# Kernel optimization log

Hardware: AMD Instinct MI355X
Metric: run time of the kernel (lower is better)

## Reference

```python
import jax, jax.numpy as jnp
import numpy as np
import math

B, T, D_MODEL, H = 2, 2048, 1024, 16
HD = D_MODEL // H  # head_dim = 64


def setup_inputs() -> dict:
    key = jax.random.key(0)
    ks = jax.random.split(key, 9)
    inp = {
        "x_q": jax.random.normal(ks[0], (B, T, D_MODEL), dtype=jnp.float32),
        "x_k": jax.random.normal(ks[1], (B, T, D_MODEL), dtype=jnp.float32),
        "x_v": jax.random.normal(ks[2], (B, T, D_MODEL), dtype=jnp.float32),
        "mask": jax.random.randint(ks[3], (B, T), 0, 2, dtype=jnp.int32),
        "causal": 1,
        "relative_position_bias": jax.random.normal(ks[4], (1, H, T, T), dtype=jnp.float32),
        "Wq": jax.random.normal(ks[5], (D_MODEL, D_MODEL), dtype=jnp.float32) * 0.02,
        "Wk": jax.random.normal(ks[6], (D_MODEL, D_MODEL), dtype=jnp.float32) * 0.02,
        "Wv": jax.random.normal(ks[7], (D_MODEL, D_MODEL), dtype=jnp.float32) * 0.02,
        "Wo": jax.random.normal(ks[8], (D_MODEL, D_MODEL), dtype=jnp.float32) * 0.02,
    }
    return inp


def _split_heads(x):
    b, t, _ = x.shape
    return x.reshape(b, t, H, HD).transpose(0, 2, 1, 3)  # (B, H, T, HD)


def reference(x_q, x_k, x_v, mask, causal, relative_position_bias, Wq, Wk, Wv, Wo):
    # torch.nn.Linear: y = x @ W.T
    q = _split_heads(x_q @ Wq.T)
    k = _split_heads(x_k @ Wk.T)
    v = _split_heads(x_v @ Wv.T)

    # padding mask (B, T_k) -> (B, 1, 1, T_k), combined with causal tril
    attn_mask = mask[:, None, None, :]
    if causal:
        tril = jnp.tril(jnp.ones((T, T), dtype=jnp.int32))[None, None]
        attn_mask = attn_mask & tril

    scores = jnp.einsum('bhqd,bhkd->bhqk', q, k) / math.sqrt(HD)
    scores = scores + relative_position_bias
    scores = jnp.where(attn_mask == 0, jnp.float32(-1e9), scores)
    attn = jax.nn.softmax(scores, axis=-1)  # (B, H, Tq, Tk)

    out_h = jnp.einsum('bhqk,bhkd->bhqd', attn, v)
    out = out_h.transpose(0, 2, 1, 3).reshape(B, T, D_MODEL)
    out = out @ Wo.T
    return out, attn
```

## Files before the change

kernel.cpp:

```cpp
#include <hip/hip_runtime.h>
#include <hip/hip_bf16.h>
#include <hip/hip_fp16.h>

#define B_ 2
#define T_ 2048
#define DM 1024
#define H_ 16
#define HD_ 64

typedef __attribute__((ext_vector_type(8))) short bf16x8v;
typedef __attribute__((ext_vector_type(4))) short short4v;
typedef __attribute__((ext_vector_type(4))) float f32x4;

__device__ __forceinline__ short f2bf(float f){
  unsigned u = __builtin_bit_cast(unsigned, f);
  u += 0x7fffu + ((u >> 16) & 1u);
  return (short)(u >> 16);
}
__device__ __forceinline__ float bf2f(short s){
  unsigned u = ((unsigned)(unsigned short)s) << 16;
  return __builtin_bit_cast(float, u);
}
__device__ __forceinline__ short f2h(float f){
  return __builtin_bit_cast(short, __float2half(f));
}
__device__ __forceinline__ float h2f(short s){
  return __half2float(__builtin_bit_cast(__half, s));
}

#define GLOAD_LDS16(g, l) \
  __builtin_amdgcn_global_load_lds((const __attribute__((address_space(1))) unsigned int*)(g), \
                                   (__attribute__((address_space(3))) unsigned int*)(l), 16, 0, 0)

#define MFMA16(a, b, c) __builtin_amdgcn_mfma_f32_16x16x32_bf16((a), (b), (c), 0, 0, 0)

__global__ __launch_bounds__(256) void conv_kernel(
    const float* __restrict__ s0, const float* __restrict__ s1, const float* __restrict__ s2,
    const float* __restrict__ s3, const float* __restrict__ s4, const float* __restrict__ s5,
    const float* __restrict__ s6,
    short* __restrict__ d0, short* __restrict__ d1, short* __restrict__ d2,
    short* __restrict__ d3, short* __restrict__ d4, short* __restrict__ d5,
    short* __restrict__ d6)
{
  int y = blockIdx.y;
  const float* s; short* d; int n;
  switch (y) {
    case 0: s = s0; d = d0; n = B_*T_*DM; break;
    case 1: s = s1; d = d1; n = B_*T_*DM; break;
    case 2: s = s2; d = d2; n = B_*T_*DM; break;
    case 3: s = s3; d = d3; n = DM*DM;   break;
    case 4: s = s4; d = d4; n = DM*DM;   break;
    case 5: s = s5; d = d5; n = DM*DM;   break;
    default: s = s6; d = d6; n = DM*DM;  break;
  }
  int i = (blockIdx.x * 256 + threadIdx.x) * 4;
  if (i >= n) return;
  float4 f = *(const float4*)(s + i);
  short4v o;
  o.x = f2bf(f.x); o.y = f2bf(f.y); o.z = f2bf(f.z); o.w = f2bf(f.w);
  *(short4v*)(d + i) = o;
}

__global__ __launch_bounds__(256) void proj_gemm(
    const short* __restrict__ xq, const short* __restrict__ xk, const short* __restrict__ xv,
    const short* __restrict__ wq, const short* __restrict__ wk, const short* __restrict__ wv,
    short* __restrict__ qo, short* __restrict__ ko, short* __restrict__ vto)
{
  __shared__ short As[128 * 32];
  __shared__ short Bs[128 * 32];
  const int z = blockIdx.z;
  const short* A  = (z == 0) ? xq : (z == 1) ? xk : xv;
  const short* Bw = (z == 0) ? wq : (z == 1) ? wk : wv;
  const int m0 = blockIdx.x * 128;
  const int n0 = blockIdx.y * 128;
  const int tid = threadIdx.x;
  const int w = tid >> 6, l = tid & 63;
  const int wr = w >> 1, wc = w & 1;
  const int fr = l & 15, kq8 = (l >> 4) * 8;
  const int srow = tid >> 2, scol = (tid & 3) * 8;

  f32x4 acc[4][4] = {};

  for (int k0 = 0; k0 < DM; k0 += 32) {
    __syncthreads();
    GLOAD_LDS16(A  + (size_t)(m0 + srow) * DM + k0 + scol,      (char*)As + tid * 16);
    GLOAD_LDS16(A  + (size_t)(m0 + 64 + srow) * DM + k0 + scol, (char*)As + 4096 + tid * 16);
    GLOAD_LDS16(Bw + (size_t)(n0 + srow) * DM + k0 + scol,      (char*)Bs + tid * 16);
    GLOAD_LDS16(Bw + (size_t)(n0 + 64 + srow) * DM + k0 + scol, (char*)Bs + 4096 + tid * 16);
    __syncthreads();
    bf16x8v a[4], b[4];
#pragma unroll
    for (int i = 0; i < 4; i++) a[i] = *(const bf16x8v*)&As[(wr * 64 + i * 16 + fr) * 32 + kq8];
#pragma unroll
    for (int j = 0; j < 4; j++) b[j] = *(const bf16x8v*)&Bs[(wc * 64 + j * 16 + fr) * 32 + kq8];
#pragma unroll
    for (int i = 0; i < 4; i++)
#pragma unroll
      for (int j = 0; j < 4; j++)
        acc[i][j] = MFMA16(a[i], b[j], acc[i][j]);
  }

  const float scale = (z == 0) ? 0.125f : 1.0f;
  short* dst01 = (z == 0) ? qo : ko;
#pragma unroll
  for (int i = 0; i < 4; i++) {
#pragma unroll
    for (int j = 0; j < 4; j++) {
#pragma unroll
      for (int r = 0; r < 4; r++) {
        int row = m0 + wr * 64 + i * 16 + (l >> 4) * 4 + r;
        int col = n0 + wc * 64 + j * 16 + fr;
        int bb = row >> 11, tt = row & (T_ - 1);
        int hh = col >> 6,  hd = col & (HD_ - 1);
        short v = f2bf(acc[i][j][r] * scale);
        if (z == 2)
          vto[(((size_t)bb * H_ + hh) * HD_ + hd) * T_ + tt] = v;
        else
          dst01[(((size_t)bb * H_ + hh) * T_ + tt) * HD_ + hd] = v;
      }
    }
  }
}

__global__ __launch_bounds__(256) void vsum_kernel(const short* __restrict__ vt,
                                                   float* __restrict__ vs)
{
  __shared__ float red[256];
  int bh = blockIdx.x;
  int tid = threadIdx.x;
  int hd = tid & 63, part = tid >> 6;
  const short* src = vt + ((size_t)bh * HD_ + hd) * T_ + part * 512;
  float s = 0.f;
  for (int i = 0; i < 512; i += 4) {
    short4v v = *(const short4v*)(src + i);
    s += bf2f(v.x) + bf2f(v.y) + bf2f(v.z) + bf2f(v.w);
  }
  red[tid] = s;
  __syncthreads();
  if (part == 0)
    vs[(size_t)bh * HD_ + hd] = red[hd] + red[64 + hd] + red[128 + hd] + red[192 + hd];
}

__global__ __launch_bounds__(512) void attn_kernel(
    const short* __restrict__ qw, const short* __restrict__ kw, const short* __restrict__ vt,
    const float* __restrict__ bias, const int* __restrict__ mask,
    const int* __restrict__ causal_p, const float* __restrict__ vsum,
    float* __restrict__ attn_out, short* __restrict__ outh)
{
  __shared__ short s_lds[32 * 2048];
  __shared__ unsigned char mk_lds[2 * T_];
  __shared__ float m_lds[32], l_lds[32];

  const int h  = blockIdx.y;
  const int q0 = blockIdx.x * 16;
  const int tid = threadIdx.x;
  const int w = tid >> 6, l = tid & 63;
  const int causal = *causal_p;
  const int L = causal ? (q0 + 16) : T_;
  const int Lpad = (L + 31) & ~31;
  const int fr = l & 15, kq8 = (l >> 4) * 8;

  for (int i = tid; i < 2 * T_; i += 512)
    mk_lds[i] = (unsigned char)(mask[i] != 0);
  __syncthreads();

  {
    bf16x8v qf[2][2];
#pragma unroll
    for (int b = 0; b < 2; b++)
#pragma unroll
      for (int ks = 0; ks < 2; ks++)
        qf[b][ks] = *(const bf16x8v*)&qw[(((size_t)b * H_ + h) * T_ + q0 + fr) * HD_ + ks * 32 + kq8];

    for (int nt = 0; nt < 16; ++nt) {
      int k0 = (nt * 8 + w) * 16;
      if (k0 >= L) break;
      f32x4 acc0 = {0.f, 0.f, 0.f, 0.f}, acc1 = {0.f, 0.f, 0.f, 0.f};
      {
        const short* kb0 = &kw[(((size_t)0 * H_ + h) * T_ + k0 + fr) * HD_ + kq8];
        acc0 = MFMA16(qf[0][0], *(const bf16x8v*)kb0, acc0);
        acc0 = MFMA16(qf[0][1], *(const bf16x8v*)(kb0 + 32), acc0);
        const short* kb1 = &kw[(((size_t)1 * H_ + h) * T_ + k0 + fr) * HD_ + kq8];
        acc1 = MFMA16(qf[1][0], *(const bf16x8v*)kb1, acc1);
        acc1 = MFMA16(qf[1][1], *(const bf16x8v*)(kb1 + 32), acc1);
      }
      int colg = k0 + fr;
      const float* bp = bias + ((size_t)h * T_ + q0 + (l >> 4) * 4) * T_ + colg;
      unsigned char mk0 = mk_lds[colg], mk1 = mk_lds[T_ + colg];
#pragma unroll
      for (int r = 0; r < 4; r++) {
        int qrel = (l >> 4) * 4 + r;
        float bi = bp[r * T_];
        bool cok = (!causal) || (colg <= q0 + qrel);
        float s0 = (mk0 && cok) ? (acc0[r] + bi) : -1e9f;
        float s1 = (mk1 && cok) ? (acc1[r] + bi) : -1e9f;
        int row0 = qrel, row1 = 16 + qrel;
        *(short*)((char*)s_lds + ((row0 * 4096 + colg * 2) ^ ((row0 & 7) << 4))) = f2h(s0);
        *(short*)((char*)s_lds + ((row1 * 4096 + colg * 2) ^ ((row1 & 7) << 4))) = f2h(s1);
      }
    }
  }
  __syncthreads();

  {
    int row = tid >> 4, j = tid & 15;
    float mx = -3e38f;
    for (int c = j * 8; c < L; c += 128) {
      int byte = (row * 4096 + c * 2) ^ ((row & 7) << 4);
      bf16x8v v = *(const bf16x8v*)((char*)s_lds + byte);
#pragma unroll
      for (int i = 0; i < 8; i++) mx = fmaxf(mx, h2f(v[i]));
    }
#pragma unroll
    for (int off = 1; off < 16; off <<= 1) mx = fmaxf(mx, __shfl_xor(mx, off));
    float sm = 0.f;
    for (int c = j * 8; c < L; c += 128) {
      int byte = (row * 4096 + c * 2) ^ ((row & 7) << 4);
      bf16x8v v = *(const bf16x8v*)((char*)s_lds + byte);
#pragma unroll
      for (int i = 0; i < 8; i++) sm += __expf(h2f(v[i]) - mx);
    }
#pragma unroll
    for (int off = 1; off < 16; off <<= 1) sm += __shfl_xor(sm, off);
    if (j == 0) { m_lds[row] = mx; l_lds[row] = sm; }
  }
  __syncthreads();

  {
    int row = tid >> 4, j = tid & 15;
    int b = row >> 4, qg = q0 + (row & 15);
    float mx = m_lds[row];
    bool fullmask = (mx <= -0.5e9f);
    float inv = fullmask ? 0.f : (1.0f / l_lds[row]);
    float fillv = fullmask ? (1.0f / (float)T_) : 0.f;
    float* arow = attn_out + (((size_t)b * H_ + h) * T_ + qg) * T_;
    for (int c = j * 8; c < Lpad; c += 128) {
      int byte = (row * 4096 + c * 2) ^ ((row & 7) << 4);
      if (c < L) {
        bf16x8v v = *(const bf16x8v*)((char*)s_lds + byte);
        float p[8];
#pragma unroll
        for (int i = 0; i < 8; i++)
          p[i] = fullmask ? 0.f : __expf(h2f(v[i]) - mx) * inv;
        float4 o0 = make_float4(fullmask ? fillv : p[0], fullmask ? fillv : p[1],
                                fullmask ? fillv : p[2], fullmask ? fillv : p[3]);
        float4 o1 = make_float4(fullmask ? fillv : p[4], fullmask ? fillv : p[5],
                                fullmask ? fillv : p[6], fullmask ? fillv : p[7]);
        *(float4*)(arow + c)     = o0;
        *(float4*)(arow + c + 4) = o1;
        bf16x8v pb;
#pragma unroll
        for (int i = 0; i < 8; i++) pb[i] = f2bf(p[i]);
        *(bf16x8v*)((char*)s_lds + byte) = pb;
      } else {
        bf16x8v zz = {0, 0, 0, 0, 0, 0, 0, 0};
        *(bf16x8v*)((char*)s_lds + byte) = zz;
      }
    }
    for (int c = L + j * 8; c < T_; c += 128) {
      float4 f4 = make_float4(fillv, fillv, fillv, fillv);
      *(float4*)(arow + c)     = f4;
      *(float4*)(arow + c + 4) = f4;
    }
  }
  __syncthreads();

  {
    int bsel = w >> 2;
    int hd0  = (w & 3) * 16;
    f32x4 acc = {0.f, 0.f, 0.f, 0.f};
    const short* vb = vt + (((size_t)bsel * H_ + h) * HD_ + hd0 + fr) * T_;
    for (int k0 = 0; k0 < Lpad; k0 += 32) {
      int arow = bsel * 16 + fr;
      int byte = (arow * 4096 + (k0 + kq8) * 2) ^ ((arow & 7) << 4);
      bf16x8v pa = *(const bf16x8v*)((char*)s_lds + byte);
      bf16x8v vv = *(const bf16x8v*)(vb + k0 + kq8);
      acc = MFMA16(pa, vv, acc);
    }
#pragma unroll
    for (int r = 0; r < 4; r++) {
      int qrel = (l >> 4) * 4 + r;
      int row = bsel * 16 + qrel;
      int hd = hd0 + fr;
      float val = acc[r];
      if (m_lds[row] <= -0.5e9f)
        val = vsum[((size_t)bsel * H_ + h) * HD_ + hd] * (1.0f / (float)T_);
      outh[(((size_t)bsel * H_ + h) * T_ + q0 + qrel) * HD_ + hd] = f2bf(val);
    }
  }
}

__global__ __launch_bounds__(256) void out_gemm(
    const short* __restrict__ Ah, const short* __restrict__ Bw, float* __restrict__ Co)
{
  __shared__ short As[128 * 32];
  __shared__ short Bs[128 * 32];
  const int m0 = blockIdx.x * 128;
  const int n0 = blockIdx.y * 128;
  const int tid = threadIdx.x;
  const int w = tid >> 6, l = tid & 63;
  const int wr = w >> 1, wc = w & 1;
  const int fr = l & 15, kq8 = (l >> 4) * 8;
  const int srow = tid >> 2, scol = (tid & 3) * 8;

  f32x4 acc[4][4] = {};

  for (int k0 = 0; k0 < DM; k0 += 32) {
    __syncthreads();
    int kk = k0 + scol;
    int hh = kk >> 6, hd = kk & 63;
    {
      int m1 = m0 + srow;
      const short* src1 = Ah + (((size_t)(m1 >> 11) * H_ + hh) * T_ + (m1 & (T_ - 1))) * HD_ + hd;
      GLOAD_LDS16(src1, (char*)As + tid * 16);
      int m2 = m0 + 64 + srow;
      const short* src2 = Ah + (((size_t)(m2 >> 11) * H_ + hh) * T_ + (m2 & (T_ - 1))) * HD_ + hd;
      GLOAD_LDS16(src2, (char*)As + 4096 + tid * 16);
    }
    GLOAD_LDS16(Bw + (size_t)(n0 + srow) * DM + kk,      (char*)Bs + tid * 16);
    GLOAD_LDS16(Bw + (size_t)(n0 + 64 + srow) * DM + kk, (char*)Bs + 4096 + tid * 16);
    __syncthreads();
    bf16x8v a[4], b[4];
#pragma unroll
    for (int i = 0; i < 4; i++) a[i] = *(const bf16x8v*)&As[(wr * 64 + i * 16 + fr) * 32 + kq8];
#pragma unroll
    for (int j = 0; j < 4; j++) b[j] = *(const bf16x8v*)&Bs[(wc * 64 + j * 16 + fr) * 32 + kq8];
#pragma unroll
    for (int i = 0; i < 4; i++)
#pragma unroll
      for (int j = 0; j < 4; j++)
        acc[i][j] = MFMA16(a[i], b[j], acc[i][j]);
  }

#pragma unroll
  for (int i = 0; i < 4; i++)
#pragma unroll
    for (int j = 0; j < 4; j++)
#pragma unroll
      for (int r = 0; r < 4; r++) {
        int row = m0 + wr * 64 + i * 16 + (l >> 4) * 4 + r;
        int col = n0 + wc * 64 + j * 16 + fr;
        Co[(size_t)row * DM + col] = acc[i][j][r];
      }
}

extern "C" void kernel_launch(void* const* d_in, const int* in_sizes, int n_in,
                              void* d_out, int out_size, void* d_ws, size_t ws_size,
                              hipStream_t stream)
{
  const float* x_q  = (const float*)d_in[0];
  const float* x_k  = (const float*)d_in[1];
  const float* x_v  = (const float*)d_in[2];
  const int*   mask = (const int*)d_in[3];
  const int*   causal = (const int*)d_in[4];
  const float* bias = (const float*)d_in[5];
  const float* Wq   = (const float*)d_in[6];
  const float* Wk   = (const float*)d_in[7];
  const float* Wv   = (const float*)d_in[8];
  const float* Wo   = (const float*)d_in[9];

  char* ws = (char*)d_ws;
  const size_t XB = (size_t)B_ * T_ * DM * 2;
  const size_t WB = (size_t)DM * DM * 2;
  short* xq_b = (short*)(ws + 0 * XB);
  short* xk_b = (short*)(ws + 1 * XB);
  short* xv_b = (short*)(ws + 2 * XB);
  short* wq_b = (short*)(ws + 3 * XB + 0 * WB);
  short* wk_b = (short*)(ws + 3 * XB + 1 * WB);
  short* wv_b = (short*)(ws + 3 * XB + 2 * WB);
  short* wo_b = (short*)(ws + 3 * XB + 3 * WB);
  short* q_ws  = (short*)(ws + 3 * XB + 4 * WB);
  short* k_ws  = (short*)(ws + 4 * XB + 4 * WB);
  short* vt_ws = (short*)(ws + 5 * XB + 4 * WB);
  short* oh_ws = (short*)(ws + 6 * XB + 4 * WB);
  float* vs_ws = (float*)(ws + 7 * XB + 4 * WB);

  float* out0 = (float*)d_out;
  float* attn = out0 + (size_t)B_ * T_ * DM;

  conv_kernel<<<dim3(4096, 7, 1), 256, 0, stream>>>(
      x_q, x_k, x_v, Wq, Wk, Wv, Wo,
      xq_b, xk_b, xv_b, wq_b, wk_b, wv_b, wo_b);

  proj_gemm<<<dim3(32, 8, 3), 256, 0, stream>>>(
      xq_b, xk_b, xv_b, wq_b, wk_b, wv_b, q_ws, k_ws, vt_ws);

  vsum_kernel<<<dim3(32, 1, 1), 256, 0, stream>>>(vt_ws, vs_ws);

  attn_kernel<<<dim3(T_ / 16, H_, 1), 512, 0, stream>>>(
      q_ws, k_ws, vt_ws, bias, mask, causal, vs_ws, attn, oh_ws);

  out_gemm<<<dim3(32, 8, 1), 256, 0, stream>>>(oh_ws, wo_b, out0);
}
```

Before: 517.2 us.

## Retile attention per batch with 8 query rows, split PV over key halves

Each attention block now covers one batch and 8 query rows instead of both batches and 16 rows, which shrinks LDS use from about 128KB to about 32KB and launches 4x as many blocks. Each wave now owns one softmax row. The PV product is split across two key halves and reduced through LDS. Attention-probability stores become nontemporal. The aim is more blocks resident per CU and better overlap of the large attn write. In exchange, half of each 16-row MFMA is wasted on duplicated rows, and the shared bias rows are no longer reused across batches within one block.

```diff
diff --git a/kernel.cpp b/kernel.cpp
--- a/kernel.cpp
+++ b/kernel.cpp
@@ -141,100 +141,94 @@
     vs[(size_t)bh * HD_ + hd] = red[hd] + red[64 + hd] + red[128 + hd] + red[192 + hd];
 }
 
-__global__ __launch_bounds__(512) void attn_kernel(
+__global__ __launch_bounds__(512, 6) void attn_kernel(
     const short* __restrict__ qw, const short* __restrict__ kw, const short* __restrict__ vt,
     const float* __restrict__ bias, const int* __restrict__ mask,
     const int* __restrict__ causal_p, const float* __restrict__ vsum,
     float* __restrict__ attn_out, short* __restrict__ outh)
 {
-  __shared__ short s_lds[32 * 2048];
-  __shared__ unsigned char mk_lds[2 * T_];
-  __shared__ float m_lds[32], l_lds[32];
-
-  const int h  = blockIdx.y;
-  const int q0 = blockIdx.x * 16;
+  __shared__ short s_lds[8 * 2048];
+  __shared__ unsigned char mk_lds[T_];
+  __shared__ float m_lds[8], l_lds[8];
+  __shared__ float pv_lds[2][8][64];
+
+  const int b  = blockIdx.x;
+  const int q0 = blockIdx.y * 8;
+  const int h  = blockIdx.z;
   const int tid = threadIdx.x;
   const int w = tid >> 6, l = tid & 63;
   const int causal = *causal_p;
-  const int L = causal ? (q0 + 16) : T_;
+  const int L = causal ? (q0 + 8) : T_;
   const int Lpad = (L + 31) & ~31;
   const int fr = l & 15, kq8 = (l >> 4) * 8;
 
-  for (int i = tid; i < 2 * T_; i += 512)
-    mk_lds[i] = (unsigned char)(mask[i] != 0);
-  __syncthreads();
-
-  {
-    bf16x8v qf[2][2];
-#pragma unroll
-    for (int b = 0; b < 2; b++)
-#pragma unroll
-      for (int ks = 0; ks < 2; ks++)
-        qf[b][ks] = *(const bf16x8v*)&qw[(((size_t)b * H_ + h) * T_ + q0 + fr) * HD_ + ks * 32 + kq8];
+  for (int i = tid; i < T_; i += 512)
+    mk_lds[i] = (unsigned char)(mask[b * T_ + i] != 0);
+  __syncthreads();
+
+  {
+    bf16x8v qf[2];
+#pragma unroll
+    for (int ks = 0; ks < 2; ks++)
+      qf[ks] = *(const bf16x8v*)&qw[(((size_t)b * H_ + h) * T_ + q0 + (fr & 7)) * HD_ + ks * 32 + kq8];
 
     for (int nt = 0; nt < 16; ++nt) {
       int k0 = (nt * 8 + w) * 16;
       if (k0 >= L) break;
-      f32x4 acc0 = {0.f, 0.f, 0.f, 0.f}, acc1 = {0.f, 0.f, 0.f, 0.f};
-      {
-        const short* kb0 = &kw[(((size_t)0 * H_ + h) * T_ + k0 + fr) * HD_ + kq8];
-        acc0 = MFMA16(qf[0][0], *(const bf16x8v*)kb0, acc0);
-        acc0 = MFMA16(qf[0][1], *(const bf16x8v*)(kb0 + 32), acc0);
-        const short* kb1 = &kw[(((size_t)1 * H_ + h) * T_ + k0 + fr) * HD_ + kq8];
-        acc1 = MFMA16(qf[1][0], *(const bf16x8v*)kb1, acc1);
-        acc1 = MFMA16(qf[1][1], *(const bf16x8v*)(kb1 + 32), acc1);
+      f32x4 acc = {0.f, 0.f, 0.f, 0.f};
+      const short* kb = &kw[(((size_t)b * H_ + h) * T_ + k0 + fr) * HD_ + kq8];
+      acc = MFMA16(qf[0], *(const bf16x8v*)kb, acc);
+      acc = MFMA16(qf[1], *(const bf16x8v*)(kb + 32), acc);
+      if ((l >> 4) < 2) {
+        int colg = k0 + fr;
+        unsigned char mk = mk_lds[colg];
+        const float* bp = bias + ((size_t)h * T_ + q0 + (l >> 4) * 4) * T_ + colg;
+#pragma unroll
+        for (int r = 0; r < 4; r++) {
+          int qrel = (l >> 4) * 4 + r;
+          float bi = bp[r * T_];
+          bool cok = (!causal) || (colg <= q0 + qrel);
+          float s = (mk && cok) ? (acc[r] + bi) : -1e9f;
+          *(short*)((char*)s_lds + ((qrel * 4096 + colg * 2) ^ ((qrel & 7) << 4))) = f2h(s);
+        }
       }
-      int colg = k0 + fr;
-      const float* bp = bias + ((size_t)h * T_ + q0 + (l >> 4) * 4) * T_ + colg;
-      unsigned char mk0 = mk_lds[colg], mk1 = mk_lds[T_ + colg];
-#pragma unroll
-      for (int r = 0; r < 4; r++) {
-        int qrel = (l >> 4) * 4 + r;
-        float bi = bp[r * T_];
-        bool cok = (!causal) || (colg <= q0 + qrel);
-        float s0 = (mk0 && cok) ? (acc0[r] + bi) : -1e9f;
-        float s1 = (mk1 && cok) ? (acc1[r] + bi) : -1e9f;
-        int row0 = qrel, row1 = 16 + qrel;
-        *(short*)((char*)s_lds + ((row0 * 4096 + colg * 2) ^ ((row0 & 7) << 4))) = f2h(s0);
-        *(short*)((char*)s_lds + ((row1 * 4096 + colg * 2) ^ ((row1 & 7) << 4))) = f2h(s1);
-      }
-    }
-  }
-  __syncthreads();
-
-  {
-    int row = tid >> 4, j = tid & 15;
+    }
+  }
+  __syncthreads();
+
+  {
+    int row = w;
     float mx = -3e38f;
-    for (int c = j * 8; c < L; c += 128) {
+    for (int c = l * 8; c < L; c += 512) {
       int byte = (row * 4096 + c * 2) ^ ((row & 7) << 4);
       bf16x8v v = *(const bf16x8v*)((char*)s_lds + byte);
 #pragma unroll
       for (int i = 0; i < 8; i++) mx = fmaxf(mx, h2f(v[i]));
     }
 #pragma unroll
-    for (int off = 1; off < 16; off <<= 1) mx = fmaxf(mx, __shfl_xor(mx, off));
+    for (int off = 1; off < 64; off <<= 1) mx = fmaxf(mx, __shfl_xor(mx, off));
     float sm = 0.f;
-    for (int c = j * 8; c < L; c += 128) {
+    for (int c = l * 8; c < L; c += 512) {
       int byte = (row * 4096 + c * 2) ^ ((row & 7) << 4);
       bf16x8v v = *(const bf16x8v*)((char*)s_lds + byte);
 #pragma unroll
       for (int i = 0; i < 8; i++) sm += __expf(h2f(v[i]) - mx);
     }
 #pragma unroll
-    for (int off = 1; off < 16; off <<= 1) sm += __shfl_xor(sm, off);
-    if (j == 0) { m_lds[row] = mx; l_lds[row] = sm; }
-  }
-  __syncthreads();
-
-  {
-    int row = tid >> 4, j = tid & 15;
-    int b = row >> 4, qg = q0 + (row & 15);
+    for (int off = 1; off < 64; off <<= 1) sm += __shfl_xor(sm, off);
+    if (l == 0) { m_lds[row] = mx; l_lds[row] = sm; }
+  }
+  __syncthreads();
+
+  {
+    int row = w;
+    int qg = q0 + row;
     float mx = m_lds[row];
     bool fullmask = (mx <= -0.5e9f);
     float inv = fullmask ? 0.f : (1.0f / l_lds[row]);
     float fillv = fullmask ? (1.0f / (float)T_) : 0.f;
     float* arow = attn_out + (((size_t)b * H_ + h) * T_ + qg) * T_;
-    for (int c = j * 8; c < Lpad; c += 128) {
+    for (int c = l * 8; c < Lpad; c += 512) {
       int byte = (row * 4096 + c * 2) ^ ((row & 7) << 4);
       if (c < L) {
         bf16x8v v = *(const bf16x8v*)((char*)s_lds + byte);
@@ -242,12 +236,12 @@
 #pragma unroll
         for (int i = 0; i < 8; i++)
           p[i] = fullmask ? 0.f : __expf(h2f(v[i]) - mx) * inv;
-        float4 o0 = make_float4(fullmask ? fillv : p[0], fullmask ? fillv : p[1],
-                                fullmask ? fillv : p[2], fullmask ? fillv : p[3]);
-        float4 o1 = make_float4(fullmask ? fillv : p[4], fullmask ? fillv : p[5],
-                                fullmask ? fillv : p[6], fullmask ? fillv : p[7]);
-        *(float4*)(arow + c)     = o0;
-        *(float4*)(arow + c + 4) = o1;
+        f32x4 o0 = {fullmask ? fillv : p[0], fullmask ? fillv : p[1],
+                    fullmask ? fillv : p[2], fullmask ? fillv : p[3]};
+        f32x4 o1 = {fullmask ? fillv : p[4], fullmask ? fillv : p[5],
+                    fullmask ? fillv : p[6], fullmask ? fillv : p[7]};
+        __builtin_nontemporal_store(o0, (f32x4*)(arow + c));
+        __builtin_nontemporal_store(o1, (f32x4*)(arow + c + 4));
         bf16x8v pb;
 #pragma unroll
         for (int i = 0; i < 8; i++) pb[i] = f2bf(p[i]);
@@ -257,36 +251,42 @@
         *(bf16x8v*)((char*)s_lds + byte) = zz;
       }
     }
-    for (int c = L + j * 8; c < T_; c += 128) {
-      float4 f4 = make_float4(fillv, fillv, fillv, fillv);
-      *(float4*)(arow + c)     = f4;
-      *(float4*)(arow + c + 4) = f4;
-    }
-  }
-  __syncthreads();
-
-  {
-    int bsel = w >> 2;
+    f32x4 f4 = {fillv, fillv, fillv, fillv};
+    for (int c = L + l * 8; c < T_; c += 512) {
+      __builtin_nontemporal_store(f4, (f32x4*)(arow + c));
+      __builtin_nontemporal_store(f4, (f32x4*)(arow + c + 4));
+    }
+  }
+  __syncthreads();
+
+  {
+    int half = w >> 2;
     int hd0  = (w & 3) * 16;
+    int split = (Lpad / 2) & ~31;
+    int kbeg = half ? split : 0;
+    int kend = half ? Lpad  : split;
     f32x4 acc = {0.f, 0.f, 0.f, 0.f};
-    const short* vb = vt + (((size_t)bsel * H_ + h) * HD_ + hd0 + fr) * T_;
-    for (int k0 = 0; k0 < Lpad; k0 += 32) {
-      int arow = bsel * 16 + fr;
+    const short* vb = vt + (((size_t)b * H_ + h) * HD_ + hd0 + fr) * T_;
+    int arow = fr & 7;
+    for (int k0 = kbeg; k0 < kend; k0 += 32) {
       int byte = (arow * 4096 + (k0 + kq8) * 2) ^ ((arow & 7) << 4);
       bf16x8v pa = *(const bf16x8v*)((char*)s_lds + byte);
       bf16x8v vv = *(const bf16x8v*)(vb + k0 + kq8);
       acc = MFMA16(pa, vv, acc);
     }
-#pragma unroll
-    for (int r = 0; r < 4; r++) {
-      int qrel = (l >> 4) * 4 + r;
-      int row = bsel * 16 + qrel;
-      int hd = hd0 + fr;
-      float val = acc[r];
-      if (m_lds[row] <= -0.5e9f)
-        val = vsum[((size_t)bsel * H_ + h) * HD_ + hd] * (1.0f / (float)T_);
-      outh[(((size_t)bsel * H_ + h) * T_ + q0 + qrel) * HD_ + hd] = f2bf(val);
-    }
+    if ((l >> 4) < 2) {
+#pragma unroll
+      for (int r = 0; r < 4; r++)
+        pv_lds[half][(l >> 4) * 4 + r][hd0 + fr] = acc[r];
+    }
+  }
+  __syncthreads();
+  {
+    int row = tid >> 6, hd = tid & 63;
+    float val = pv_lds[0][row][hd] + pv_lds[1][row][hd];
+    if (m_lds[row] <= -0.5e9f)
+      val = vsum[((size_t)b * H_ + h) * HD_ + hd] * (1.0f / (float)T_);
+    outh[(((size_t)b * H_ + h) * T_ + q0 + row) * HD_ + hd] = f2bf(val);
   }
 }
 
@@ -387,7 +387,7 @@
 
   vsum_kernel<<<dim3(32, 1, 1), 256, 0, stream>>>(vt_ws, vs_ws);
 
-  attn_kernel<<<dim3(T_ / 16, H_, 1), 512, 0, stream>>>(
+  attn_kernel<<<dim3(B_, T_ / 8, H_), 512, 0, stream>>>(
       q_ws, k_ws, vt_ws, bias, mask, causal, vs_ws, attn, oh_ws);
 
   out_gemm<<<dim3(32, 8, 1), 256, 0, stream>>>(oh_ws, wo_b, out0);
```

Result: faster. 463.3 us (-10.4%).
